# Optimization experiments

Measured on AMD Instinct MI355X. Metric: run time of the kernel, lower is better.

## Reference

```python
import jax, jax.numpy as jnp
import numpy as np

B, NP, PS, D = 4, 512, 16, 1024
NH = 4            # intra attention heads
HD = D // NH      # intra head dim
PH = 4            # pool heads
PHD = D // PH     # pool head dim
K = 5             # depthwise conv kernel size


def _rms_norm(x):
    # F.rms_norm with eps=None -> eps = finfo(dtype).eps, no learned weight
    eps = jnp.finfo(x.dtype).eps
    return x * jax.lax.rsqrt(jnp.mean(x * x, axis=-1, keepdims=True) + eps)


def setup_inputs() -> dict:
    key = jax.random.key(0)
    ks = jax.random.split(key, 12)
    s = 0.02
    return {
        "patch_byte_emb": jax.random.normal(ks[0], (B, NP, PS, D), jnp.float32),
        "local_pos": jax.random.normal(ks[1], (PS, D), jnp.float32) * 0.01,
        "w_gate": jax.random.normal(ks[2], (D, D), jnp.float32) * s,
        "w_in": jax.random.normal(ks[3], (D, D), jnp.float32) * s,
        "conv_w": jax.random.normal(ks[4], (D, 1, K), jnp.float32) * s,  # depthwise (out=D, in/groups=1, k)
        "w_qkv": jax.random.normal(ks[5], (3 * D, D), jnp.float32) * s,
        "w_intra_out": jax.random.normal(ks[6], (D, D), jnp.float32) * s,
        "w_pool": jax.random.normal(ks[7], (PH, D), jnp.float32) * s,
        "attn_temperature": jnp.ones((1,), jnp.float32),
        "w_up": jax.random.normal(ks[8], (D, D), jnp.float32) * s,
        "w_down": jax.random.normal(ks[9], (D, D), jnp.float32) * s,
        "w_out": jax.random.normal(ks[10], (D, D), jnp.float32) * s,
    }


def reference(patch_byte_emb, local_pos, w_gate, w_in, conv_w, w_qkv,
              w_intra_out, w_pool, attn_temperature, w_up, w_down, w_out):
    x = patch_byte_emb + local_pos[None, None]            # [B,NP,PS,D]
    x = _rms_norm(x)
    # SiLU-gated projection (CastedLinear: y = x @ W.T, no bias)
    x = jax.nn.silu(x @ w_gate.T) * (x @ w_in.T)
    bsz, num_patches, patch_size, model_dim = x.shape

    # depthwise causal-style conv1d: padding=4 both sides, then keep first PS outputs
    x_flat = x.reshape(bsz * num_patches, patch_size, model_dim).transpose(0, 2, 1)  # [BN,D,PS]
    conv_out = jax.lax.conv_general_dilated(
        x_flat, conv_w, window_strides=(1,), padding=[(K - 1, K - 1)],
        feature_group_count=model_dim,
        dimension_numbers=("NCH", "OIH", "NCH"))[:, :, :patch_size]
    x = x + conv_out.transpose(0, 2, 1).reshape(bsz, num_patches, patch_size, model_dim)

    # tiny per-patch self-attention
    x_sa = _rms_norm(x).reshape(bsz * num_patches, patch_size, model_dim)
    qkv = (x_sa @ w_qkv.T).reshape(bsz * num_patches, patch_size, 3, NH, HD)
    q, k, v = qkv[:, :, 0], qkv[:, :, 1], qkv[:, :, 2]    # [BN,PS,NH,HD]
    attn = jnp.einsum("bqhd,bkhd->bhqk", q, k) * (HD ** -0.5)
    attn = jax.nn.softmax(attn, axis=-1)
    sa = jnp.einsum("bhqk,bkhd->bqhd", attn, v).reshape(bsz * num_patches, patch_size, model_dim)
    x = x + (sa @ w_intra_out.T).reshape(bsz, num_patches, patch_size, model_dim)

    # multi-head attention pooling over patch positions
    x = _rms_norm(x)
    temp = jnp.clip(attn_temperature, 0.01, None).astype(x.dtype)  # [1]
    attn_logits = (x @ w_pool.T) / temp                   # [B,NP,PS,PH]
    attn_w = jax.nn.softmax(attn_logits.transpose(0, 1, 3, 2), axis=-1)  # [B,NP,PH,PS]
    x_heads = x.reshape(bsz, num_patches, patch_size, PH, PHD)
    pooled = jnp.einsum("bnhp,bnphd->bnhd", attn_w, x_heads).reshape(bsz, num_patches, model_dim)

    # post MLP + out proj
    y = pooled + (jax.nn.silu(_rms_norm(pooled) @ w_up.T) @ w_down.T)
    y = y @ w_out.T
    return _rms_norm(y)
```

## Files before the change

kernel.cpp:

```cpp
#include <hip/hip_runtime.h>
#include <cstdint>
#include <cstddef>


typedef __bf16 bf16x8 __attribute__((ext_vector_type(8)));
typedef float floatx4 __attribute__((ext_vector_type(4)));

#define DEV static __device__ __forceinline__

DEV unsigned short f2bf(float f) {
  union { float f; unsigned u; } x; x.f = f;
  unsigned r = x.u + 0x7fffu + ((x.u >> 16) & 1u);
  return (unsigned short)(r >> 16);
}
DEV float bf2f(unsigned short b) {
  union { unsigned u; float f; } x; x.u = ((unsigned)b) << 16;
  return x.f;
}
DEV float silu_f(float v) { return v / (1.f + __expf(-v)); }

DEV void gl_lds16(const unsigned short* g, unsigned short* l) {
  __builtin_amdgcn_global_load_lds(
      (const __attribute__((address_space(1))) void*)g,
      (__attribute__((address_space(3))) void*)l, 16, 0, 0);
}

DEV float block_reduce_sum(float v) {
  #pragma unroll
  for (int o = 32; o > 0; o >>= 1) v += __shfl_down(v, o, 64);
  __shared__ float s[4];
  int w = threadIdx.x >> 6;
  if ((threadIdx.x & 63) == 0) s[w] = v;
  __syncthreads();
  return s[0] + s[1] + s[2] + s[3];
}

struct CvtArgs {
  const float* src[7];
  unsigned short* dst[7];
  int blkoff[8];
};
__global__ __launch_bounds__(256) void cvt_all(CvtArgs a) {
  int b = blockIdx.x;
  int w = 0;
  #pragma unroll
  for (int i = 0; i < 6; i++) w += (b >= a.blkoff[i + 1]) ? 1 : 0;
  int i = (b - a.blkoff[w]) * 1024 + threadIdx.x * 4;
  float4 v = *(const float4*)(a.src[w] + i);
  ushort4 o;
  o.x = f2bf(v.x); o.y = f2bf(v.y); o.z = f2bf(v.z); o.w = f2bf(v.w);
  *(ushort4*)(a.dst[w] + i) = o;
}

__global__ __launch_bounds__(256) void prep_kernel(const float* __restrict__ pbe,
                                                   const float* __restrict__ pos,
                                                   unsigned short* __restrict__ xn) {
  int row = blockIdx.x;
  int t = row & 15;
  const float* ip = pbe + (size_t)row * 1024;
  const float* pp = pos + (size_t)t * 1024;
  int c = threadIdx.x * 4;
  float4 v = *(const float4*)(ip + c);
  float4 p = *(const float4*)(pp + c);
  v.x += p.x; v.y += p.y; v.z += p.z; v.w += p.w;
  float ss = v.x * v.x + v.y * v.y + v.z * v.z + v.w * v.w;
  ss = block_reduce_sum(ss);
  float sc = rsqrtf(ss * (1.f / 1024.f) + 1.1920929e-7f);
  ushort4 o;
  o.x = f2bf(v.x * sc); o.y = f2bf(v.y * sc); o.z = f2bf(v.z * sc); o.w = f2bf(v.w * sc);
  *(ushort4*)(xn + (size_t)row * 1024 + c) = o;
}

DEV float ldval(const float* p, size_t i) { return p[i]; }
DEV float ldval(const unsigned short* p, size_t i) { return bf2f(p[i]); }
DEV void stval(float* p, size_t i, float v) { p[i] = v; }
DEV void stval(unsigned short* p, size_t i, float v) { p[i] = f2bf(v); }

template <typename TI, typename TO>
__global__ __launch_bounds__(256) void rmsnorm_kernel(const TI* __restrict__ in,
                                                      TO* __restrict__ out) {
  size_t row = blockIdx.x;
  const TI* ip = in + row * 1024;
  TO* op = out + row * 1024;
  int c = threadIdx.x * 4;
  float v[4]; float ss = 0.f;
  #pragma unroll
  for (int j = 0; j < 4; j++) { v[j] = ldval(ip, c + j); ss += v[j] * v[j]; }
  ss = block_reduce_sum(ss);
  float sc = rsqrtf(ss * (1.f / 1024.f) + 1.1920929e-7f);
  #pragma unroll
  for (int j = 0; j < 4; j++) stval(op, c + j, v[j] * sc);
}


template <int R>
DEV void stage_rows(const unsigned short* __restrict__ src, int ldK,
                    unsigned short* lds, int k0, int wave, int lane) {
  constexpr int PER_WAVE = R / 32;
  #pragma unroll
  for (int d = 0; d < PER_WAVE; d++) {
    int di = wave * PER_WAVE + d;
    int r = di * 8 + (lane >> 3);
    int c = (lane & 7) ^ (r & 7);
    gl_lds16(src + (size_t)r * ldK + k0 + c * 8, lds + di * 512);
  }
}
DEV int frag_off64(int row, int g) {
  return row * 64 + ((g ^ (row & 7)) * 8);
}

template <int EPI, int TM, int TN>
__global__ __launch_bounds__(256) void gemm_bt(
    const unsigned short* __restrict__ A, const unsigned short* __restrict__ Bw,
    int M, int N, int K,
    float* __restrict__ outF, unsigned short* __restrict__ outB,
    const unsigned short* __restrict__ resB, const float* __restrict__ resF) {
  constexpr int AI = TM / 32;
  constexpr int BJ = TN / 32;
  __shared__ __align__(16) unsigned short As[TM * 64];
  __shared__ __align__(16) unsigned short Bs[TN * 64];
  const int tid = threadIdx.x;
  const int bm = blockIdx.y * TM, bn = blockIdx.x * TN;
  const int wave = tid >> 6, lane = tid & 63;
  const int wy = wave >> 1, wx = wave & 1;
  const int l15 = lane & 15, quad = lane >> 4;

  floatx4 acc[AI][BJ];
  #pragma unroll
  for (int i = 0; i < AI; i++)
    #pragma unroll
    for (int j = 0; j < BJ; j++)
      #pragma unroll
      for (int r = 0; r < 4; r++) acc[i][j][r] = 0.f;

  const unsigned short* Ab = A + (size_t)bm * K;
  const unsigned short* Bb = Bw + (size_t)bn * K;
  int arow[AI], brow[BJ];
  #pragma unroll
  for (int i = 0; i < AI; i++) arow[i] = wy * (TM / 2) + i * 16 + l15;
  #pragma unroll
  for (int j = 0; j < BJ; j++) brow[j] = wx * (TN / 2) + j * 16 + l15;

  for (int k0 = 0; k0 < K; k0 += 64) {
    __syncthreads();
    stage_rows<TM>(Ab, K, As, k0, wave, lane);
    stage_rows<TN>(Bb, K, Bs, k0, wave, lane);
    __syncthreads();
    #pragma unroll
    for (int h = 0; h < 2; h++) {
      bf16x8 afr[AI], bfr[BJ];
      #pragma unroll
      for (int i = 0; i < AI; i++) afr[i] = *(const bf16x8*)&As[frag_off64(arow[i], h * 4 + quad)];
      #pragma unroll
      for (int j = 0; j < BJ; j++) bfr[j] = *(const bf16x8*)&Bs[frag_off64(brow[j], h * 4 + quad)];
      #pragma unroll
      for (int i = 0; i < AI; i++)
        #pragma unroll
        for (int j = 0; j < BJ; j++)
          acc[i][j] = __builtin_amdgcn_mfma_f32_16x16x32_bf16(afr[i], bfr[j], acc[i][j], 0, 0, 0);
    }
  }

  #pragma unroll
  for (int i = 0; i < AI; i++)
    #pragma unroll
    for (int j = 0; j < BJ; j++) {
      int gm = bm + wy * (TM / 2) + i * 16 + quad * 4;
      int gn = bn + wx * (TN / 2) + j * 16 + l15;
      #pragma unroll
      for (int r = 0; r < 4; r++) {
        float v = acc[i][j][r];
        size_t idx = (size_t)(gm + r) * N + gn;
        if (EPI == 0) outF[idx] = v;
        else if (EPI == 1) outB[idx] = f2bf(v);
        else if (EPI == 2) outB[idx] = f2bf(silu_f(v));
        else if (EPI == 3) outB[idx] = f2bf(v + bf2f(resB[idx]));
        else if (EPI == 4) outB[idx] = f2bf(v + resF[idx]);
      }
    }
}

__global__ __launch_bounds__(256) void gemm_dual(
    const unsigned short* __restrict__ A, const unsigned short* __restrict__ Bg,
    const unsigned short* __restrict__ Bi, int M, int N, int K,
    unsigned short* __restrict__ outH) {
  __shared__ __align__(16) unsigned short As[128 * 64];
  __shared__ __align__(16) unsigned short Gs[64 * 64];
  __shared__ __align__(16) unsigned short Is[64 * 64];
  const int tid = threadIdx.x;
  const int bm = blockIdx.y * 128, bn = blockIdx.x * 64;
  const int wave = tid >> 6, lane = tid & 63;
  const int wy = wave >> 1, wx = wave & 1;
  const int l15 = lane & 15, quad = lane >> 4;

  floatx4 accg[4][2], acci[4][2];
  #pragma unroll
  for (int i = 0; i < 4; i++)
    #pragma unroll
    for (int j = 0; j < 2; j++)
      #pragma unroll
      for (int r = 0; r < 4; r++) { accg[i][j][r] = 0.f; acci[i][j][r] = 0.f; }

  const unsigned short* Ab = A + (size_t)bm * K;
  const unsigned short* Gb = Bg + (size_t)bn * K;
  const unsigned short* Ib = Bi + (size_t)bn * K;
  int arow[4], brow[2];
  #pragma unroll
  for (int i = 0; i < 4; i++) arow[i] = wy * 64 + i * 16 + l15;
  #pragma unroll
  for (int j = 0; j < 2; j++) brow[j] = wx * 32 + j * 16 + l15;

  for (int k0 = 0; k0 < K; k0 += 64) {
    __syncthreads();
    stage_rows<128>(Ab, K, As, k0, wave, lane);
    stage_rows<64>(Gb, K, Gs, k0, wave, lane);
    stage_rows<64>(Ib, K, Is, k0, wave, lane);
    __syncthreads();
    #pragma unroll
    for (int h = 0; h < 2; h++) {
      bf16x8 afr[4], gfr[2], ifr[2];
      #pragma unroll
      for (int i = 0; i < 4; i++) afr[i] = *(const bf16x8*)&As[frag_off64(arow[i], h * 4 + quad)];
      #pragma unroll
      for (int j = 0; j < 2; j++) {
        gfr[j] = *(const bf16x8*)&Gs[frag_off64(brow[j], h * 4 + quad)];
        ifr[j] = *(const bf16x8*)&Is[frag_off64(brow[j], h * 4 + quad)];
      }
      #pragma unroll
      for (int i = 0; i < 4; i++)
        #pragma unroll
        for (int j = 0; j < 2; j++) {
          accg[i][j] = __builtin_amdgcn_mfma_f32_16x16x32_bf16(afr[i], gfr[j], accg[i][j], 0, 0, 0);
          acci[i][j] = __builtin_amdgcn_mfma_f32_16x16x32_bf16(afr[i], ifr[j], acci[i][j], 0, 0, 0);
        }
    }
  }

  #pragma unroll
  for (int i = 0; i < 4; i++)
    #pragma unroll
    for (int j = 0; j < 2; j++) {
      int gm = bm + wy * 64 + i * 16 + quad * 4;
      int gn = bn + wx * 32 + j * 16 + l15;
      #pragma unroll
      for (int r = 0; r < 4; r++) {
        size_t idx = (size_t)(gm + r) * N + gn;
        outH[idx] = f2bf(silu_f(accg[i][j][r]) * acci[i][j][r]);
      }
    }
}

#define HS_LD 1040
__global__ __launch_bounds__(256) void conv_rms_kernel(const unsigned short* __restrict__ h,
                                                       const float* __restrict__ cw,
                                                       unsigned short* __restrict__ x2,
                                                       unsigned short* __restrict__ x2n) {
  int patch = blockIdx.x;
  __shared__ __align__(16) unsigned short hs[16 * HS_LD];
  __shared__ __align__(16) float cwp[5 * 1024];
  const int tid = threadIdx.x;
  size_t base = (size_t)patch * 16384;
  for (int idx = tid * 8; idx < 16384; idx += 256 * 8) {
    int row = idx >> 10, col = idx & 1023;
    *(uint4*)&hs[row * HS_LD + col] = *(const uint4*)&h[base + idx];
  }
  for (int i = tid; i < 5120; i += 256) {
    int c = i / 5, k = i - c * 5;
    cwp[k * 1024 + c] = cw[i];
  }
  __syncthreads();
  int t = tid >> 4;
  int lc = (tid & 15) * 8;
  float vals[8][8];
  float ss = 0.f;
  #pragma unroll
  for (int jb = 0; jb < 8; jb++) {
    int c = jb * 128 + lc;
    float tap[5][8];
    #pragma unroll
    for (int k = 0; k < 5; k++) {
      int tt = t + k - 4;
      if (tt >= 0) {
        uint4 v = *(const uint4*)&hs[tt * HS_LD + c];
        const unsigned short* vp = (const unsigned short*)&v;
        #pragma unroll
        for (int i = 0; i < 8; i++) tap[k][i] = bf2f(vp[i]);
      } else {
        #pragma unroll
        for (int i = 0; i < 8; i++) tap[k][i] = 0.f;
      }
    }
    float w[5][8];
    #pragma unroll
    for (int k = 0; k < 5; k++) {
      float4 a = *(const float4*)&cwp[k * 1024 + c];
      float4 b = *(const float4*)&cwp[k * 1024 + c + 4];
      w[k][0] = a.x; w[k][1] = a.y; w[k][2] = a.z; w[k][3] = a.w;
      w[k][4] = b.x; w[k][5] = b.y; w[k][6] = b.z; w[k][7] = b.w;
    }
    #pragma unroll
    for (int i = 0; i < 8; i++) {
      float acc = tap[4][i];
      #pragma unroll
      for (int k = 0; k < 5; k++) acc += w[k][i] * tap[k][i];
      vals[jb][i] = acc;
      ss += acc * acc;
    }
  }
  ss += __shfl_down(ss, 8, 16);
  ss += __shfl_down(ss, 4, 16);
  ss += __shfl_down(ss, 2, 16);
  ss += __shfl_down(ss, 1, 16);
  ss = __shfl(ss, 0, 16);
  float sc = rsqrtf(ss * (1.f / 1024.f) + 1.1920929e-7f);
  #pragma unroll
  for (int jb = 0; jb < 8; jb++) {
    ushort4 o2[2], on[2];
    #pragma unroll
    for (int i = 0; i < 8; i++) {
      ((unsigned short*)o2)[i] = f2bf(vals[jb][i]);
      ((unsigned short*)on)[i] = f2bf(vals[jb][i] * sc);
    }
    size_t off = base + (size_t)t * 1024 + jb * 128 + lc;
    *(uint4*)&x2[off] = *(uint4*)o2;
    *(uint4*)&x2n[off] = *(uint4*)on;
  }
}

__global__ __launch_bounds__(256) void attn_kernel(const unsigned short* __restrict__ qkv,
                                                   unsigned short* __restrict__ sa) {
  int patch = blockIdx.x;
  int head = blockIdx.y;
  const int tid = threadIdx.x;
  __shared__ float qs[16][260], ks[16][260], vs[16][260];
  __shared__ float sc[16][16];
  size_t base = (size_t)patch * 16 * 3072 + (size_t)head * 256;
  for (int idx = tid * 8; idx < 16 * 256; idx += 256 * 8) {
    int t = idx >> 8, d = idx & 255;
    size_t roff = base + (size_t)t * 3072 + d;
    uint4 qv = *(const uint4*)&qkv[roff];
    uint4 kv = *(const uint4*)&qkv[roff + 1024];
    uint4 vv = *(const uint4*)&qkv[roff + 2048];
    const unsigned short* qp = (const unsigned short*)&qv;
    const unsigned short* kp = (const unsigned short*)&kv;
    const unsigned short* vp = (const unsigned short*)&vv;
    #pragma unroll
    for (int i = 0; i < 8; i++) {
      qs[t][d + i] = bf2f(qp[i]);
      ks[t][d + i] = bf2f(kp[i]);
      vs[t][d + i] = bf2f(vp[i]);
    }
  }
  __syncthreads();
  {
    int t = tid >> 4, kk = tid & 15;
    float s = 0.f;
    for (int d = 0; d < 256; d += 4) {
      float4 q = *(const float4*)&qs[t][d];
      float4 k = *(const float4*)&ks[kk][d];
      s += q.x * k.x + q.y * k.y + q.z * k.z + q.w * k.w;
    }
    sc[t][kk] = s * 0.0625f;
  }
  __syncthreads();
  if (tid < 16) {
    float m = -1e30f;
    for (int kk = 0; kk < 16; kk++) m = fmaxf(m, sc[tid][kk]);
    float p[16], sum = 0.f;
    for (int kk = 0; kk < 16; kk++) { p[kk] = __expf(sc[tid][kk] - m); sum += p[kk]; }
    float inv = 1.f / sum;
    for (int kk = 0; kk < 16; kk++) sc[tid][kk] = p[kk] * inv;
  }
  __syncthreads();
  for (int idx = tid * 8; idx < 4096; idx += 256 * 8) {
    int t = idx >> 8, d = idx & 255;
    float o[8] = {0, 0, 0, 0, 0, 0, 0, 0};
    #pragma unroll
    for (int kk = 0; kk < 16; kk++) {
      float w = sc[t][kk];
      float4 v0 = *(const float4*)&vs[kk][d];
      float4 v1 = *(const float4*)&vs[kk][d + 4];
      o[0] += w * v0.x; o[1] += w * v0.y; o[2] += w * v0.z; o[3] += w * v0.w;
      o[4] += w * v1.x; o[5] += w * v1.y; o[6] += w * v1.z; o[7] += w * v1.w;
    }
    ushort4 ov[2];
    #pragma unroll
    for (int i = 0; i < 8; i++) ((unsigned short*)ov)[i] = f2bf(o[i]);
    *(uint4*)&sa[(size_t)(patch * 16 + t) * 1024 + head * 256 + d] = *(uint4*)ov;
  }
}

__global__ __launch_bounds__(256) void pool_kernel(const unsigned short* __restrict__ x4,
                                                   const float* __restrict__ wpool,
                                                   const float* __restrict__ tptr,
                                                   float* __restrict__ pooled,
                                                   unsigned short* __restrict__ pooledn) {
  int patch = blockIdx.x;
  __shared__ __align__(16) unsigned short xs[16 * 1024];
  __shared__ float lg[4][16], aw[4][16];
  const int tid = threadIdx.x;
  size_t base = (size_t)patch * 16384;
  for (int idx = tid * 8; idx < 16384; idx += 256 * 8)
    *(uint4*)&xs[idx] = *(const uint4*)&x4[base + idx];
  __syncthreads();
  {
    int pair = tid >> 2, sub = tid & 3;
    int t = pair >> 2, hh = pair & 3;
    float s = 0.f;
    for (int d = sub * 256; d < sub * 256 + 256; d++)
      s += bf2f(xs[t * 1024 + d]) * wpool[hh * 1024 + d];
    s += __shfl_down(s, 2, 64);
    s += __shfl_down(s, 1, 64);
    if (sub == 0) {
      float temp = fmaxf(tptr[0], 0.01f);
      lg[hh][t] = s / temp;
    }
  }
  __syncthreads();
  if (tid < 4) {
    int hh = tid;
    float m = -1e30f;
    for (int t = 0; t < 16; t++) m = fmaxf(m, lg[hh][t]);
    float p[16], sum = 0.f;
    for (int t = 0; t < 16; t++) { p[t] = __expf(lg[hh][t] - m); sum += p[t]; }
    float inv = 1.f / sum;
    for (int t = 0; t < 16; t++) aw[hh][t] = p[t] * inv;
  }
  __syncthreads();
  float ov[4]; int cs[4];
  float ss = 0.f;
  #pragma unroll
  for (int q = 0; q < 4; q++) {
    int c = tid + q * 256;
    int hh = c >> 8;
    float o = 0.f;
    #pragma unroll
    for (int t = 0; t < 16; t++) o += aw[hh][t] * bf2f(xs[t * 1024 + c]);
    ov[q] = o; cs[q] = c;
    ss += o * o;
  }
  ss = block_reduce_sum(ss);
  float scn = rsqrtf(ss * (1.f / 1024.f) + 1.1920929e-7f);
  #pragma unroll
  for (int q = 0; q < 4; q++) {
    pooled[(size_t)patch * 1024 + cs[q]] = ov[q];
    pooledn[(size_t)patch * 1024 + cs[q]] = f2bf(ov[q] * scn);
  }
}

extern "C" void kernel_launch(void* const* d_in, const int* in_sizes, int n_in,
                              void* d_out, int out_size, void* d_ws, size_t ws_size,
                              hipStream_t stream) {
  (void)in_sizes; (void)n_in; (void)out_size; (void)ws_size;
  const float* pbe  = (const float*)d_in[0];
  const float* lpos = (const float*)d_in[1];
  const float* wg   = (const float*)d_in[2];
  const float* wi   = (const float*)d_in[3];
  const float* cw   = (const float*)d_in[4];
  const float* wqkv = (const float*)d_in[5];
  const float* wio  = (const float*)d_in[6];
  const float* wpl  = (const float*)d_in[7];
  const float* temp = (const float*)d_in[8];
  const float* wup  = (const float*)d_in[9];
  const float* wdn  = (const float*)d_in[10];
  const float* wout = (const float*)d_in[11];
  float* outp = (float*)d_out;

  const int ROWS = 32768, Dm = 1024, NPAT = 2048;

  char* p = (char*)d_ws;
  auto take = [&](size_t nbytes) { void* r = (void*)p; p += (nbytes + 255) & ~(size_t)255; return r; };
  unsigned short* wg_b   = (unsigned short*)take((size_t)Dm * Dm * 2);
  unsigned short* wi_b   = (unsigned short*)take((size_t)Dm * Dm * 2);
  unsigned short* wqkv_b = (unsigned short*)take((size_t)3 * Dm * Dm * 2);
  unsigned short* wio_b  = (unsigned short*)take((size_t)Dm * Dm * 2);
  unsigned short* wup_b  = (unsigned short*)take((size_t)Dm * Dm * 2);
  unsigned short* wdn_b  = (unsigned short*)take((size_t)Dm * Dm * 2);
  unsigned short* wout_b = (unsigned short*)take((size_t)Dm * Dm * 2);
  unsigned short* slotA  = (unsigned short*)take((size_t)ROWS * Dm * 2);
  unsigned short* slotB  = (unsigned short*)take((size_t)ROWS * Dm * 2);
  unsigned short* slotC  = (unsigned short*)take((size_t)ROWS * Dm * 2);
  unsigned short* qkvB   = (unsigned short*)take((size_t)ROWS * 3 * Dm * 2);
  float*          pooled = (float*)take((size_t)NPAT * Dm * 4);
  unsigned short* pooledn= (unsigned short*)take((size_t)NPAT * Dm * 2);
  unsigned short* ubuf   = (unsigned short*)take((size_t)NPAT * Dm * 2);
  unsigned short* y1b    = (unsigned short*)take((size_t)NPAT * Dm * 2);
  float*          y2     = (float*)take((size_t)NPAT * Dm * 4);

  CvtArgs ca;
  ca.src[0] = wg;   ca.dst[0] = wg_b;
  ca.src[1] = wi;   ca.dst[1] = wi_b;
  ca.src[2] = wqkv; ca.dst[2] = wqkv_b;
  ca.src[3] = wio;  ca.dst[3] = wio_b;
  ca.src[4] = wup;  ca.dst[4] = wup_b;
  ca.src[5] = wdn;  ca.dst[5] = wdn_b;
  ca.src[6] = wout; ca.dst[6] = wout_b;
  int off = 0;
  for (int i = 0; i < 7; i++) { ca.blkoff[i] = off; off += (i == 2) ? 3072 : 1024; }
  ca.blkoff[7] = off;
  cvt_all<<<dim3(off), dim3(256), 0, stream>>>(ca);

  prep_kernel<<<dim3(ROWS), dim3(256), 0, stream>>>(pbe, lpos, slotA);
  gemm_dual<<<dim3(Dm / 64, ROWS / 128), dim3(256), 0, stream>>>(
      slotA, wg_b, wi_b, ROWS, Dm, Dm, slotB);
  conv_rms_kernel<<<dim3(NPAT), dim3(256), 0, stream>>>(slotB, cw, slotC, slotA);
  gemm_bt<1, 128, 128><<<dim3(3 * Dm / 128, ROWS / 128), dim3(256), 0, stream>>>(
      slotA, wqkv_b, ROWS, 3 * Dm, Dm, nullptr, qkvB, nullptr, nullptr);
  attn_kernel<<<dim3(NPAT, 4), dim3(256), 0, stream>>>(qkvB, slotB);
  gemm_bt<3, 128, 128><<<dim3(Dm / 128, ROWS / 128), dim3(256), 0, stream>>>(
      slotB, wio_b, ROWS, Dm, Dm, nullptr, slotC, slotC, nullptr);
  rmsnorm_kernel<unsigned short, unsigned short><<<dim3(ROWS), dim3(256), 0, stream>>>(slotC, slotA);
  pool_kernel<<<dim3(NPAT), dim3(256), 0, stream>>>(slotA, wpl, temp, pooled, pooledn);
  gemm_bt<2, 64, 128><<<dim3(Dm / 128, NPAT / 64), dim3(256), 0, stream>>>(
      pooledn, wup_b, NPAT, Dm, Dm, nullptr, ubuf, nullptr, nullptr);
  gemm_bt<4, 64, 128><<<dim3(Dm / 128, NPAT / 64), dim3(256), 0, stream>>>(
      ubuf, wdn_b, NPAT, Dm, Dm, nullptr, y1b, nullptr, pooled);
  gemm_bt<0, 64, 128><<<dim3(Dm / 128, NPAT / 64), dim3(256), 0, stream>>>(
      y1b, wout_b, NPAT, Dm, Dm, y2, nullptr, nullptr, nullptr);
  rmsnorm_kernel<float, float><<<dim3(NPAT), dim3(256), 0, stream>>>(y2, outp);
}
```

Baseline: 1.141 ms.

## Warp-specialize GEMMs with double-buffered LDS and fold RMSNorm into pooling

All GEMM kernels now run 512 threads, with 4 producer waves that stage the next K-tile into a second LDS buffer while 4 consumer waves run MFMAs on the current one. This needs one barrier per iteration instead of two. Separately, the standalone RMSNorm before pooling is removed, and its per-row scale is computed inside pool_kernel and applied to the logits and the pooled sum. The GEMM change doubles LDS use, and the producer waves only issue loads, which may reduce occupancy. There is also a risk that async global_load_lds writes are not complete when the barrier is reached.

```diff
diff --git a/kernel.cpp b/kernel.cpp
--- a/kernel.cpp
+++ b/kernel.cpp
@@ -95,11 +95,11 @@
 
 template <int R>
 DEV void stage_rows(const unsigned short* __restrict__ src, int ldK,
-                    unsigned short* lds, int k0, int wave, int lane) {
+                    unsigned short* lds, int k0, int pw, int lane) {
   constexpr int PER_WAVE = R / 32;
   #pragma unroll
   for (int d = 0; d < PER_WAVE; d++) {
-    int di = wave * PER_WAVE + d;
+    int di = pw * PER_WAVE + d;
     int r = di * 8 + (lane >> 3);
     int c = (lane & 7) ^ (r & 7);
     gl_lds16(src + (size_t)r * ldK + k0 + c * 8, lds + di * 512);
@@ -110,57 +110,74 @@
 }
 
 template <int EPI, int TM, int TN>
-__global__ __launch_bounds__(256) void gemm_bt(
+__global__ __launch_bounds__(512) void gemm_ws(
     const unsigned short* __restrict__ A, const unsigned short* __restrict__ Bw,
     int M, int N, int K,
     float* __restrict__ outF, unsigned short* __restrict__ outB,
     const unsigned short* __restrict__ resB, const float* __restrict__ resF) {
   constexpr int AI = TM / 32;
   constexpr int BJ = TN / 32;
-  __shared__ __align__(16) unsigned short As[TM * 64];
-  __shared__ __align__(16) unsigned short Bs[TN * 64];
+  __shared__ __align__(16) unsigned short As[2][TM * 64];
+  __shared__ __align__(16) unsigned short Bs[2][TN * 64];
   const int tid = threadIdx.x;
   const int bm = blockIdx.y * TM, bn = blockIdx.x * TN;
   const int wave = tid >> 6, lane = tid & 63;
-  const int wy = wave >> 1, wx = wave & 1;
+  const bool producer = wave >= 4;
+  const int pw = wave & 3;
+  const int wy = (wave & 3) >> 1, wx = wave & 1;
   const int l15 = lane & 15, quad = lane >> 4;
-
-  floatx4 acc[AI][BJ];
-  #pragma unroll
-  for (int i = 0; i < AI; i++)
-    #pragma unroll
-    for (int j = 0; j < BJ; j++)
-      #pragma unroll
-      for (int r = 0; r < 4; r++) acc[i][j][r] = 0.f;
 
   const unsigned short* Ab = A + (size_t)bm * K;
   const unsigned short* Bb = Bw + (size_t)bn * K;
+
+  floatx4 acc[AI][BJ];
+  #pragma unroll
+  for (int i = 0; i < AI; i++)
+    #pragma unroll
+    for (int j = 0; j < BJ; j++)
+      #pragma unroll
+      for (int r = 0; r < 4; r++) acc[i][j][r] = 0.f;
+
   int arow[AI], brow[BJ];
   #pragma unroll
   for (int i = 0; i < AI; i++) arow[i] = wy * (TM / 2) + i * 16 + l15;
   #pragma unroll
   for (int j = 0; j < BJ; j++) brow[j] = wx * (TN / 2) + j * 16 + l15;
 
-  for (int k0 = 0; k0 < K; k0 += 64) {
+  const int iters = K >> 6;
+  if (producer) {
+    stage_rows<TM>(Ab, K, As[0], 0, pw, lane);
+    stage_rows<TN>(Bb, K, Bs[0], 0, pw, lane);
+  }
+  __syncthreads();
+  for (int it = 0; it < iters; ++it) {
+    const int cur = it & 1;
+    if (producer) {
+      if (it + 1 < iters) {
+        stage_rows<TM>(Ab, K, As[cur ^ 1], (it + 1) << 6, pw, lane);
+        stage_rows<TN>(Bb, K, Bs[cur ^ 1], (it + 1) << 6, pw, lane);
+      }
+    } else {
+      #pragma unroll
+      for (int h = 0; h < 2; h++) {
+        bf16x8 afr[AI], bfr[BJ];
+        #pragma unroll
+        for (int i = 0; i < AI; i++)
+          afr[i] = *(const bf16x8*)&As[cur][frag_off64(arow[i], h * 4 + quad)];
+        #pragma unroll
+        for (int j = 0; j < BJ; j++)
+          bfr[j] = *(const bf16x8*)&Bs[cur][frag_off64(brow[j], h * 4 + quad)];
+        #pragma unroll
+        for (int i = 0; i < AI; i++)
+          #pragma unroll
+          for (int j = 0; j < BJ; j++)
+            acc[i][j] = __builtin_amdgcn_mfma_f32_16x16x32_bf16(afr[i], bfr[j], acc[i][j], 0, 0, 0);
+      }
+    }
     __syncthreads();
-    stage_rows<TM>(Ab, K, As, k0, wave, lane);
-    stage_rows<TN>(Bb, K, Bs, k0, wave, lane);
-    __syncthreads();
-    #pragma unroll
-    for (int h = 0; h < 2; h++) {
-      bf16x8 afr[AI], bfr[BJ];
-      #pragma unroll
-      for (int i = 0; i < AI; i++) afr[i] = *(const bf16x8*)&As[frag_off64(arow[i], h * 4 + quad)];
-      #pragma unroll
-      for (int j = 0; j < BJ; j++) bfr[j] = *(const bf16x8*)&Bs[frag_off64(brow[j], h * 4 + quad)];
-      #pragma unroll
-      for (int i = 0; i < AI; i++)
-        #pragma unroll
-        for (int j = 0; j < BJ; j++)
-          acc[i][j] = __builtin_amdgcn_mfma_f32_16x16x32_bf16(afr[i], bfr[j], acc[i][j], 0, 0, 0);
-    }
-  }
-
+  }
+
+  if (producer) return;
   #pragma unroll
   for (int i = 0; i < AI; i++)
     #pragma unroll
@@ -180,62 +197,79 @@
     }
 }
 
-__global__ __launch_bounds__(256) void gemm_dual(
+__global__ __launch_bounds__(512) void gemm_dual_ws(
     const unsigned short* __restrict__ A, const unsigned short* __restrict__ Bg,
     const unsigned short* __restrict__ Bi, int M, int N, int K,
     unsigned short* __restrict__ outH) {
-  __shared__ __align__(16) unsigned short As[128 * 64];
-  __shared__ __align__(16) unsigned short Gs[64 * 64];
-  __shared__ __align__(16) unsigned short Is[64 * 64];
+  __shared__ __align__(16) unsigned short As[2][128 * 64];
+  __shared__ __align__(16) unsigned short Gs[2][64 * 64];
+  __shared__ __align__(16) unsigned short Is[2][64 * 64];
   const int tid = threadIdx.x;
   const int bm = blockIdx.y * 128, bn = blockIdx.x * 64;
   const int wave = tid >> 6, lane = tid & 63;
-  const int wy = wave >> 1, wx = wave & 1;
+  const bool producer = wave >= 4;
+  const int pw = wave & 3;
+  const int wy = (wave & 3) >> 1, wx = wave & 1;
   const int l15 = lane & 15, quad = lane >> 4;
-
-  floatx4 accg[4][2], acci[4][2];
-  #pragma unroll
-  for (int i = 0; i < 4; i++)
-    #pragma unroll
-    for (int j = 0; j < 2; j++)
-      #pragma unroll
-      for (int r = 0; r < 4; r++) { accg[i][j][r] = 0.f; acci[i][j][r] = 0.f; }
 
   const unsigned short* Ab = A + (size_t)bm * K;
   const unsigned short* Gb = Bg + (size_t)bn * K;
   const unsigned short* Ib = Bi + (size_t)bn * K;
+
+  floatx4 accg[4][2], acci[4][2];
+  #pragma unroll
+  for (int i = 0; i < 4; i++)
+    #pragma unroll
+    for (int j = 0; j < 2; j++)
+      #pragma unroll
+      for (int r = 0; r < 4; r++) { accg[i][j][r] = 0.f; acci[i][j][r] = 0.f; }
+
   int arow[4], brow[2];
   #pragma unroll
   for (int i = 0; i < 4; i++) arow[i] = wy * 64 + i * 16 + l15;
   #pragma unroll
   for (int j = 0; j < 2; j++) brow[j] = wx * 32 + j * 16 + l15;
 
-  for (int k0 = 0; k0 < K; k0 += 64) {
+  const int iters = K >> 6;
+  if (producer) {
+    stage_rows<128>(Ab, K, As[0], 0, pw, lane);
+    stage_rows<64>(Gb, K, Gs[0], 0, pw, lane);
+    stage_rows<64>(Ib, K, Is[0], 0, pw, lane);
+  }
+  __syncthreads();
+  for (int it = 0; it < iters; ++it) {
+    const int cur = it & 1;
+    if (producer) {
+      if (it + 1 < iters) {
+        stage_rows<128>(Ab, K, As[cur ^ 1], (it + 1) << 6, pw, lane);
+        stage_rows<64>(Gb, K, Gs[cur ^ 1], (it + 1) << 6, pw, lane);
+        stage_rows<64>(Ib, K, Is[cur ^ 1], (it + 1) << 6, pw, lane);
+      }
+    } else {
+      #pragma unroll
+      for (int h = 0; h < 2; h++) {
+        bf16x8 afr[4], gfr[2], ifr[2];
+        #pragma unroll
+        for (int i = 0; i < 4; i++)
+          afr[i] = *(const bf16x8*)&As[cur][frag_off64(arow[i], h * 4 + quad)];
+        #pragma unroll
+        for (int j = 0; j < 2; j++) {
+          gfr[j] = *(const bf16x8*)&Gs[cur][frag_off64(brow[j], h * 4 + quad)];
+          ifr[j] = *(const bf16x8*)&Is[cur][frag_off64(brow[j], h * 4 + quad)];
+        }
+        #pragma unroll
+        for (int i = 0; i < 4; i++)
+          #pragma unroll
+          for (int j = 0; j < 2; j++) {
+            accg[i][j] = __builtin_amdgcn_mfma_f32_16x16x32_bf16(afr[i], gfr[j], accg[i][j], 0, 0, 0);
+            acci[i][j] = __builtin_amdgcn_mfma_f32_16x16x32_bf16(afr[i], ifr[j], acci[i][j], 0, 0, 0);
+          }
+      }
+    }
     __syncthreads();
-    stage_rows<128>(Ab, K, As, k0, wave, lane);
-    stage_rows<64>(Gb, K, Gs, k0, wave, lane);
-    stage_rows<64>(Ib, K, Is, k0, wave, lane);
-    __syncthreads();
-    #pragma unroll
-    for (int h = 0; h < 2; h++) {
-      bf16x8 afr[4], gfr[2], ifr[2];
-      #pragma unroll
-      for (int i = 0; i < 4; i++) afr[i] = *(const bf16x8*)&As[frag_off64(arow[i], h * 4 + quad)];
-      #pragma unroll
-      for (int j = 0; j < 2; j++) {
-        gfr[j] = *(const bf16x8*)&Gs[frag_off64(brow[j], h * 4 + quad)];
-        ifr[j] = *(const bf16x8*)&Is[frag_off64(brow[j], h * 4 + quad)];
-      }
-      #pragma unroll
-      for (int i = 0; i < 4; i++)
-        #pragma unroll
-        for (int j = 0; j < 2; j++) {
-          accg[i][j] = __builtin_amdgcn_mfma_f32_16x16x32_bf16(afr[i], gfr[j], accg[i][j], 0, 0, 0);
-          acci[i][j] = __builtin_amdgcn_mfma_f32_16x16x32_bf16(afr[i], ifr[j], acci[i][j], 0, 0, 0);
-        }
-    }
-  }
-
+  }
+
+  if (producer) return;
   #pragma unroll
   for (int i = 0; i < 4; i++)
     #pragma unroll
@@ -390,18 +424,34 @@
   }
 }
 
-__global__ __launch_bounds__(256) void pool_kernel(const unsigned short* __restrict__ x4,
+__global__ __launch_bounds__(256) void pool_kernel(const unsigned short* __restrict__ x3,
                                                    const float* __restrict__ wpool,
                                                    const float* __restrict__ tptr,
                                                    float* __restrict__ pooled,
                                                    unsigned short* __restrict__ pooledn) {
   int patch = blockIdx.x;
   __shared__ __align__(16) unsigned short xs[16 * 1024];
-  __shared__ float lg[4][16], aw[4][16];
+  __shared__ float lg[4][16], aw[4][16], srow[16];
   const int tid = threadIdx.x;
   size_t base = (size_t)patch * 16384;
   for (int idx = tid * 8; idx < 16384; idx += 256 * 8)
-    *(uint4*)&xs[idx] = *(const uint4*)&x4[base + idx];
+    *(uint4*)&xs[idx] = *(const uint4*)&x3[base + idx];
+  __syncthreads();
+  {
+    int t = tid >> 4, sub = tid & 15;
+    float ss = 0.f;
+    for (int d = sub * 64; d < sub * 64 + 64; d += 4) {
+      uint2 v = *(const uint2*)&xs[t * 1024 + d];
+      const unsigned short* vp = (const unsigned short*)&v;
+      #pragma unroll
+      for (int i = 0; i < 4; i++) { float x = bf2f(vp[i]); ss += x * x; }
+    }
+    ss += __shfl_down(ss, 8, 16);
+    ss += __shfl_down(ss, 4, 16);
+    ss += __shfl_down(ss, 2, 16);
+    ss += __shfl_down(ss, 1, 16);
+    if (sub == 0) srow[t] = rsqrtf(ss * (1.f / 1024.f) + 1.1920929e-7f);
+  }
   __syncthreads();
   {
     int pair = tid >> 2, sub = tid & 3;
@@ -413,7 +463,7 @@
     s += __shfl_down(s, 1, 64);
     if (sub == 0) {
       float temp = fmaxf(tptr[0], 0.01f);
-      lg[hh][t] = s / temp;
+      lg[hh][t] = s * srow[t] / temp;
     }
   }
   __syncthreads();
@@ -435,7 +485,7 @@
     int hh = c >> 8;
     float o = 0.f;
     #pragma unroll
-    for (int t = 0; t < 16; t++) o += aw[hh][t] * bf2f(xs[t * 1024 + c]);
+    for (int t = 0; t < 16; t++) o += aw[hh][t] * srow[t] * bf2f(xs[t * 1024 + c]);
     ov[q] = o; cs[q] = c;
     ss += o * o;
   }
@@ -501,21 +551,20 @@
   cvt_all<<<dim3(off), dim3(256), 0, stream>>>(ca);
 
   prep_kernel<<<dim3(ROWS), dim3(256), 0, stream>>>(pbe, lpos, slotA);
-  gemm_dual<<<dim3(Dm / 64, ROWS / 128), dim3(256), 0, stream>>>(
+  gemm_dual_ws<<<dim3(Dm / 64, ROWS / 128), dim3(512), 0, stream>>>(
       slotA, wg_b, wi_b, ROWS, Dm, Dm, slotB);
   conv_rms_kernel<<<dim3(NPAT), dim3(256), 0, stream>>>(slotB, cw, slotC, slotA);
-  gemm_bt<1, 128, 128><<<dim3(3 * Dm / 128, ROWS / 128), dim3(256), 0, stream>>>(
+  gemm_ws<1, 128, 128><<<dim3(3 * Dm / 128, ROWS / 128), dim3(512), 0, stream>>>(
       slotA, wqkv_b, ROWS, 3 * Dm, Dm, nullptr, qkvB, nullptr, nullptr);
   attn_kernel<<<dim3(NPAT, 4), dim3(256), 0, stream>>>(qkvB, slotB);
-  gemm_bt<3, 128, 128><<<dim3(Dm / 128, ROWS / 128), dim3(256), 0, stream>>>(
+  gemm_ws<3, 128, 128><<<dim3(Dm / 128, ROWS / 128), dim3(512), 0, stream>>>(
       slotB, wio_b, ROWS, Dm, Dm, nullptr, slotC, slotC, nullptr);
-  rmsnorm_kernel<unsigned short, unsigned short><<<dim3(ROWS), dim3(256), 0, stream>>>(slotC, slotA);
-  pool_kernel<<<dim3(NPAT), dim3(256), 0, stream>>>(slotA, wpl, temp, pooled, pooledn);
-  gemm_bt<2, 64, 128><<<dim3(Dm / 128, NPAT / 64), dim3(256), 0, stream>>>(
+  pool_kernel<<<dim3(NPAT), dim3(256), 0, stream>>>(slotC, wpl, temp, pooled, pooledn);
+  gemm_ws<2, 64, 128><<<dim3(Dm / 128, NPAT / 64), dim3(512), 0, stream>>>(
       pooledn, wup_b, NPAT, Dm, Dm, nullptr, ubuf, nullptr, nullptr);
-  gemm_bt<4, 64, 128><<<dim3(Dm / 128, NPAT / 64), dim3(256), 0, stream>>>(
+  gemm_ws<4, 64, 128><<<dim3(Dm / 128, NPAT / 64), dim3(512), 0, stream>>>(
       ubuf, wdn_b, NPAT, Dm, Dm, nullptr, y1b, nullptr, pooled);
-  gemm_bt<0, 64, 128><<<dim3(Dm / 128, NPAT / 64), dim3(256), 0, stream>>>(
+  gemm_ws<0, 64, 128><<<dim3(Dm / 128, NPAT / 64), dim3(512), 0, stream>>>(
       y1b, wout_b, NPAT, Dm, Dm, y2, nullptr, nullptr, nullptr);
   rmsnorm_kernel<float, float><<<dim3(NPAT), dim3(256), 0, stream>>>(y2, outp);
 }
```

New measurement: 1.074 ms. 5.8% less time.
